# Kernel optimization log

Measured on AMD Instinct MI355X. Metric: run time of the kernel, lower is better.

## Reference

```python
import jax, jax.numpy as jnp
import numpy as np

N_NODES = 4096
N_EDGES = 131072
NUM_USERS = 50000
NUM_ITEMS = 50000
EMB = 64
NUM_CLASSES = 41476
BN_EPS = 1e-5


def _seg_sum(x, idx, n):
    return jax.ops.segment_sum(x, idx, num_segments=n)


def gcn_conv(x, ei, W, b):
    # PyG GCNConv: linear, add self-loops, sym norm D^-1/2 (A+I) D^-1/2, sum-agg, +bias
    n = x.shape[0]
    h = x @ W
    loop = jnp.arange(n, dtype=ei.dtype)
    row = jnp.concatenate([ei[0], loop])
    col = jnp.concatenate([ei[1], loop])
    deg = _seg_sum(jnp.ones_like(col, h.dtype), col, n)
    dinv = jnp.where(deg > 0, deg ** -0.5, 0.0)
    norm = dinv[row] * dinv[col]
    return _seg_sum(h[row] * norm[:, None], col, n) + b


def sage_conv(x, ei, Wl, bl, Wr):
    # PyG SAGEConv (mean aggr): mean_neighbors(x) @ Wl + bl + x @ Wr
    n = x.shape[0]
    ones = jnp.ones((ei.shape[1],), x.dtype)
    cnt = _seg_sum(ones, ei[1], n)
    agg = _seg_sum(x[ei[0]], ei[1], n) / jnp.maximum(cnt, 1.0)[:, None]
    return agg @ Wl + bl + x @ Wr


def cheb_conv(x, ei, W0, W1, b):
    # PyG ChebConv K=2, sym norm, lambda_max=2: L_hat = L - I = -D^-1/2 A D^-1/2
    # out = x @ W0 + (L_hat x) @ W1 + b
    n = x.shape[0]
    ones = jnp.ones((ei.shape[1],), x.dtype)
    deg = _seg_sum(ones, ei[0], n)  # row-sum degree (get_laplacian)
    dinv = jnp.where(deg > 0, deg ** -0.5, 0.0)
    w = -(dinv[ei[0]] * dinv[ei[1]])
    tx1 = _seg_sum(x[ei[0]] * w[:, None], ei[1], n)
    return x @ W0 + tx1 @ W1 + b


def gat_conv(x, ei, W, a_src, a_dst, b):
    # PyG GATConv heads=1, concat=False, self-loops added, leaky_relu(0.2) + softmax over in-edges
    n = x.shape[0]
    h = x @ W
    loop = jnp.arange(n, dtype=ei.dtype)
    row = jnp.concatenate([ei[0], loop])
    col = jnp.concatenate([ei[1], loop])
    a_s = h @ a_src  # [n]
    a_d = h @ a_dst
    e = jax.nn.leaky_relu(a_s[row] + a_d[col], 0.2)
    emax = jax.ops.segment_max(e, col, num_segments=n)  # every segment nonempty (self-loops)
    ex = jnp.exp(e - emax[col])
    denom = _seg_sum(ex, col, n)
    alpha = ex / denom[col]
    return _seg_sum(h[row] * alpha[:, None], col, n) + b


def batch_norm(x, g, be):
    mu = jnp.mean(x, axis=0)
    var = jnp.var(x, axis=0)
    return (x - mu) * jax.lax.rsqrt(var + BN_EPS) * g + be


def setup_inputs() -> dict:
    key = jax.random.key(0)
    ks = iter(jax.random.split(key, 48))
    nrm = lambda shape, s=0.05: jax.random.normal(next(ks), shape, jnp.float32) * s
    edge_index = jax.random.randint(next(ks), (2, N_EDGES), 0, N_NODES, jnp.int32)
    node_x = jax.random.randint(next(ks), (N_NODES, 2), 0, NUM_USERS, jnp.int32)
    inp = dict(
        edge_index=edge_index, node_x=node_x,
        user_emb_w=nrm((NUM_USERS, EMB)), item_emb_w=nrm((NUM_ITEMS, EMB)),
        mlp_w1=nrm((2 * EMB, 1024)), mlp_b1=jnp.zeros((1024,), jnp.float32),
        mlp_w2=nrm((1024, 512)), mlp_b2=jnp.zeros((512,), jnp.float32),
        gcn_w1=nrm((512, 256)), gcn_b1=jnp.zeros((256,), jnp.float32),
        bn1_g=jnp.ones((256,), jnp.float32), bn1_b=jnp.zeros((256,), jnp.float32),
        gcn_w2=nrm((256, 128)), gcn_b2=jnp.zeros((128,), jnp.float32),
        bn2_g=jnp.ones((128,), jnp.float32), bn2_b=jnp.zeros((128,), jnp.float32),
        sage_wl=nrm((128, 128)), sage_bl=jnp.zeros((128,), jnp.float32), sage_wr=nrm((128, 128)),
        cheb_w0=nrm((128, 128)), cheb_w1=nrm((128, 128)), cheb_b=jnp.zeros((128,), jnp.float32),
        gat1_w=nrm((128, 128)), gat1_asrc=nrm((128,)), gat1_adst=nrm((128,)), gat1_b=jnp.zeros((128,), jnp.float32),
        gat2_w=nrm((128, 128)), gat2_asrc=nrm((128,)), gat2_adst=nrm((128,)), gat2_b=jnp.zeros((128,), jnp.float32),
        pred_w=nrm((128, NUM_CLASSES)), pred_b=jnp.zeros((NUM_CLASSES,), jnp.float32),
    )
    return inp


def reference(edge_index, node_x, user_emb_w, item_emb_w, mlp_w1, mlp_b1, mlp_w2, mlp_b2,
              gcn_w1, gcn_b1, bn1_g, bn1_b, gcn_w2, gcn_b2, bn2_g, bn2_b,
              sage_wl, sage_bl, sage_wr, cheb_w0, cheb_w1, cheb_b,
              gat1_w, gat1_asrc, gat1_adst, gat1_b, gat2_w, gat2_asrc, gat2_adst, gat2_b,
              pred_w, pred_b):
    u = user_emb_w[node_x[:, 0]]
    i = item_emb_w[node_x[:, 1]]
    x = jnp.concatenate([u, i], axis=1)  # [N, 2*EMB]
    x = jax.nn.relu(x @ mlp_w1 + mlp_b1)  # dropout = identity (eval mode)
    x = jax.nn.relu(x @ mlp_w2 + mlp_b2)
    x = jax.nn.relu(batch_norm(gcn_conv(x, edge_index, gcn_w1, gcn_b1), bn1_g, bn1_b))
    x = jax.nn.relu(batch_norm(gcn_conv(x, edge_index, gcn_w2, gcn_b2), bn2_g, bn2_b))
    x = jax.nn.relu(sage_conv(x, edge_index, sage_wl, sage_bl, sage_wr))
    x = jax.nn.relu(cheb_conv(x, edge_index, cheb_w0, cheb_w1, cheb_b))
    x = jax.nn.elu(gat_conv(x, edge_index, gat1_w, gat1_asrc, gat1_adst, gat1_b))
    x = jax.nn.elu(gat_conv(x, edge_index, gat2_w, gat2_asrc, gat2_adst, gat2_b))
    return x @ pred_w + pred_b  # [N, NUM_CLASSES]
```

## Files before the change

### kernel.cpp

```cpp
#include <hip/hip_runtime.h>
#include <math.h>

#define NN 4096
#define NE 131072
#define NCLS 41476
#define NPAD 41600

typedef __attribute__((ext_vector_type(8))) unsigned short ushort8;
typedef __attribute__((ext_vector_type(8))) __bf16 bf16x8;
typedef __attribute__((ext_vector_type(4))) float f32x4;

__device__ __forceinline__ unsigned short f2bf(float f) {
  unsigned u = __float_as_uint(f);
  unsigned r = u + 0x7fffu + ((u >> 16) & 1u);
  return (unsigned short)(r >> 16);
}
__device__ __forceinline__ float bf2f(unsigned short u) {
  return __uint_as_float(((unsigned)u) << 16);
}

struct CvtDesc { const float* src; unsigned short* dst; int K, N, ld, koff, tile0, ntx; };
struct CvtArgs { CvtDesc d[11]; };

__global__ void k_fused0(CvtArgs a, int cvtBlocks, const int* __restrict__ ei,
                         int* __restrict__ deg0, int* __restrict__ deg1,
                         const int* __restrict__ node_x, const float* __restrict__ uw,
                         const float* __restrict__ iw, unsigned short* __restrict__ x0) {
  int b = blockIdx.x;
  int tid = threadIdx.x;
  if (b < cvtBlocks) {
    __shared__ float s[32][33];
    int di = 0;
#pragma unroll
    for (int i = 1; i < 11; i++)
      if (a.d[i].tile0 <= b) di = i;
    const CvtDesc dd = a.d[di];
    int t = b - dd.tile0;
    int n0 = (t % dd.ntx) * 32, k0 = (t / dd.ntx) * 32;
    int c = tid & 31, r8 = tid >> 5;
#pragma unroll
    for (int r = 0; r < 4; r++) {
      int k = k0 + r8 + r * 8, n = n0 + c;
      s[r8 + r * 8][c] = (n < dd.N) ? dd.src[(size_t)k * dd.N + n] : 0.f;
    }
    __syncthreads();
#pragma unroll
    for (int r = 0; r < 4; r++) {
      int n = n0 + r8 + r * 8, k = k0 + c;
      dd.dst[(size_t)n * dd.ld + dd.koff + k] = f2bf(s[c][r8 + r * 8]);
    }
  } else if (b < cvtBlocks + 512) {
    int bid = b - cvtBlocks;
    for (int i = bid * 256 + tid; i < 2 * NE; i += 512 * 256) {
      int v = ei[i];
      atomicAdd((i < NE ? deg0 : deg1) + v, 1);
    }
  } else {
    int nb = b - cvtBlocks - 512;
    int n = nb * 2 + (tid >> 7);
    int t = tid & 127;
    int u = node_x[n * 2], it = node_x[n * 2 + 1];
    float v = (t < 64) ? uw[u * 64 + t] : iw[it * 64 + (t - 64)];
    x0[n * 128 + t] = f2bf(v);
  }
}

template <int OUTBF>
__global__ __launch_bounds__(256) void k_bgemm(const unsigned short* __restrict__ A,
                                               const unsigned short* __restrict__ Bt,
                                               const float* __restrict__ bias,
                                               void* __restrict__ Cv, int N, int K, int relu) {
  __shared__ unsigned short As[128 * 128];
  __shared__ unsigned short Bs[128 * 128];
  int m0 = blockIdx.y * 128;
  int n0 = blockIdx.x * 128;
  int tid = threadIdx.x;
  int wave = tid >> 6, lane = tid & 63;
  int wm = (wave >> 1) * 64, wn = (wave & 1) * 64;
  int lr = lane & 15, lg = lane >> 4;
  f32x4 acc[4][4] = {};
  for (int k0 = 0; k0 < K; k0 += 128) {
#pragma unroll
    for (int i = 0; i < 8; i++) {
      int idx = tid + i * 256;
      int row = idx >> 4, ku = idx & 15;
      int sw = (ku ^ (row & 7)) * 8;
      *reinterpret_cast<ushort8*>(As + row * 128 + sw) =
          *reinterpret_cast<const ushort8*>(A + (size_t)(m0 + row) * K + k0 + ku * 8);
      *reinterpret_cast<ushort8*>(Bs + row * 128 + sw) =
          *reinterpret_cast<const ushort8*>(Bt + (size_t)(n0 + row) * K + k0 + ku * 8);
    }
    __syncthreads();
#pragma unroll
    for (int kk = 0; kk < 4; kk++) {
      bf16x8 af[4], bfr[4];
#pragma unroll
      for (int mi = 0; mi < 4; mi++) {
        int row = wm + mi * 16 + lr;
        af[mi] = __builtin_bit_cast(
            bf16x8, *reinterpret_cast<const ushort8*>(As + row * 128 + (((kk * 4 + lg) ^ (row & 7)) * 8)));
        int col = wn + mi * 16 + lr;
        bfr[mi] = __builtin_bit_cast(
            bf16x8, *reinterpret_cast<const ushort8*>(Bs + col * 128 + (((kk * 4 + lg) ^ (col & 7)) * 8)));
      }
#pragma unroll
      for (int mi = 0; mi < 4; mi++)
#pragma unroll
        for (int ni = 0; ni < 4; ni++)
          acc[mi][ni] = __builtin_amdgcn_mfma_f32_16x16x32_bf16(af[mi], bfr[ni], acc[mi][ni], 0, 0, 0);
    }
    __syncthreads();
  }
#pragma unroll
  for (int mi = 0; mi < 4; mi++) {
#pragma unroll
    for (int ni = 0; ni < 4; ni++) {
      int col = n0 + wn + ni * 16 + lr;
      if (col < N) {
        float bv = bias ? bias[col] : 0.f;
#pragma unroll
        for (int r = 0; r < 4; r++) {
          int row = m0 + wm + mi * 16 + lg * 4 + r;
          float v = acc[mi][ni][r] + bv;
          if (relu) v = fmaxf(v, 0.f);
          if (OUTBF)
            ((unsigned short*)Cv)[(size_t)row * N + col] = f2bf(v);
          else
            ((float*)Cv)[(size_t)row * N + col] = v;
        }
      }
    }
  }
}

__global__ __launch_bounds__(256) void k_pred_gemm(const unsigned short* __restrict__ A,
                                                   const unsigned short* __restrict__ Bt,
                                                   const float* __restrict__ bias,
                                                   float* __restrict__ C) {
  __shared__ unsigned short As[128 * 128];
  __shared__ unsigned short Bs[128 * 128];
  int n0 = blockIdx.x * 128;
  int tid = threadIdx.x;
  int wave = tid >> 6, lane = tid & 63;
  int wm = (wave >> 1) * 64, wn = (wave & 1) * 64;
  int lr = lane & 15, lg = lane >> 4;
#pragma unroll
  for (int i = 0; i < 8; i++) {
    int idx = tid + i * 256;
    int row = idx >> 4, ku = idx & 15;
    int sw = (ku ^ (row & 7)) * 8;
    *reinterpret_cast<ushort8*>(Bs + row * 128 + sw) =
        *reinterpret_cast<const ushort8*>(Bt + (size_t)(n0 + row) * 128 + ku * 8);
  }
  float bv[4];
  int colv[4];
#pragma unroll
  for (int ni = 0; ni < 4; ni++) {
    colv[ni] = n0 + wn + ni * 16 + lr;
    bv[ni] = (colv[ni] < NCLS) ? bias[colv[ni]] : 0.f;
  }
  int mt0 = blockIdx.y * 8;
  for (int mt = mt0; mt < mt0 + 8; ++mt) {
    int m0 = mt * 128;
    __syncthreads();
#pragma unroll
    for (int i = 0; i < 8; i++) {
      int idx = tid + i * 256;
      int row = idx >> 4, ku = idx & 15;
      int sw = (ku ^ (row & 7)) * 8;
      *reinterpret_cast<ushort8*>(As + row * 128 + sw) =
          *reinterpret_cast<const ushort8*>(A + (size_t)(m0 + row) * 128 + ku * 8);
    }
    __syncthreads();
    f32x4 acc[4][4] = {};
#pragma unroll
    for (int kk = 0; kk < 4; kk++) {
      bf16x8 af[4], bfr[4];
#pragma unroll
      for (int mi = 0; mi < 4; mi++) {
        int row = wm + mi * 16 + lr;
        af[mi] = __builtin_bit_cast(
            bf16x8, *reinterpret_cast<const ushort8*>(As + row * 128 + (((kk * 4 + lg) ^ (row & 7)) * 8)));
        int col = wn + mi * 16 + lr;
        bfr[mi] = __builtin_bit_cast(
            bf16x8, *reinterpret_cast<const ushort8*>(Bs + col * 128 + (((kk * 4 + lg) ^ (col & 7)) * 8)));
      }
#pragma unroll
      for (int mi = 0; mi < 4; mi++)
#pragma unroll
        for (int ni = 0; ni < 4; ni++)
          acc[mi][ni] = __builtin_amdgcn_mfma_f32_16x16x32_bf16(af[mi], bfr[ni], acc[mi][ni], 0, 0, 0);
    }
#pragma unroll
    for (int mi = 0; mi < 4; mi++) {
#pragma unroll
      for (int ni = 0; ni < 4; ni++) {
        if (colv[ni] < NCLS) {
#pragma unroll
          for (int r = 0; r < 4; r++) {
            int row = m0 + wm + mi * 16 + lg * 4 + r;
            C[(size_t)row * NCLS + colv[ni]] = acc[mi][ni][r] + bv[ni];
          }
        }
      }
    }
  }
}

template <int MODE>
__global__ __launch_bounds__(256) void k_bgemm_s(const void* __restrict__ Av,
                                                 const unsigned short* __restrict__ Bt,
                                                 const float* __restrict__ bias,
                                                 unsigned short* __restrict__ C, int ldC,
                                                 int K, int relu,
                                                 const float* __restrict__ psum,
                                                 const float* __restrict__ psq,
                                                 const float* __restrict__ bng,
                                                 const float* __restrict__ bnb,
                                                 const float* __restrict__ asrc,
                                                 const float* __restrict__ adst,
                                                 float* __restrict__ o_as,
                                                 float* __restrict__ o_ad) {
  __shared__ unsigned short As[32 * 64];
  __shared__ unsigned short Bs[128 * 64];
  __shared__ float sc[256], sh[256];
  __shared__ float sas[4][32], sad[4][32];
  int m0 = blockIdx.y * 32;
  int n0 = blockIdx.x * 128;
  int tid = threadIdx.x;
  int wave = tid >> 6, lane = tid & 63;
  int wn = wave * 32;
  int lr = lane & 15, lg = lane >> 4;
  if (MODE == 1) {
    if (tid < K) {
      int S = 16384 / K;
      float s = 0.f, s2 = 0.f;
      for (int i = 0; i < S; i++) {
        s += psum[(size_t)i * K + tid];
        s2 += psq[(size_t)i * K + tid];
      }
      float invM = 1.f / (float)NN;
      float mu = s * invM;
      float var = s2 * invM - mu * mu;
      float scv = bng[tid] * rsqrtf(var + 1e-5f);
      sc[tid] = scv;
      sh[tid] = bnb[tid] - mu * scv;
    }
    __syncthreads();
  }
  f32x4 acc[2][2] = {};
  for (int k0 = 0; k0 < K; k0 += 64) {
    {
      int row = tid >> 3, uu = tid & 7, sw = (uu ^ (row & 7)) * 8;
      if (MODE == 1) {
        const float* Af = (const float*)Av;
        const float* p = Af + (size_t)(m0 + row) * K + k0 + uu * 8;
        float4 p0 = *reinterpret_cast<const float4*>(p);
        float4 p1 = *reinterpret_cast<const float4*>(p + 4);
        int kb = k0 + uu * 8;
        float pv[8] = {p0.x, p0.y, p0.z, p0.w, p1.x, p1.y, p1.z, p1.w};
        ushort8 o;
#pragma unroll
        for (int j = 0; j < 8; j++) o[j] = f2bf(fmaxf(pv[j] * sc[kb + j] + sh[kb + j], 0.f));
        *reinterpret_cast<ushort8*>(As + row * 64 + sw) = o;
      } else {
        *reinterpret_cast<ushort8*>(As + row * 64 + sw) =
            *reinterpret_cast<const ushort8*>((const unsigned short*)Av + (size_t)(m0 + row) * K + k0 + uu * 8);
      }
    }
#pragma unroll
    for (int i = 0; i < 4; i++) {
      int idx = tid + i * 256;
      int row = idx >> 3, uu = idx & 7, sw = (uu ^ (row & 7)) * 8;
      *reinterpret_cast<ushort8*>(Bs + row * 64 + sw) =
          *reinterpret_cast<const ushort8*>(Bt + (size_t)(n0 + row) * K + k0 + uu * 8);
    }
    __syncthreads();
#pragma unroll
    for (int kk = 0; kk < 2; kk++) {
      bf16x8 af[2], bfr[2];
#pragma unroll
      for (int mi = 0; mi < 2; mi++) {
        int row = mi * 16 + lr;
        af[mi] = __builtin_bit_cast(
            bf16x8, *reinterpret_cast<const ushort8*>(As + row * 64 + (((kk * 4 + lg) ^ (row & 7)) * 8)));
        int col = wn + mi * 16 + lr;
        bfr[mi] = __builtin_bit_cast(
            bf16x8, *reinterpret_cast<const ushort8*>(Bs + col * 64 + (((kk * 4 + lg) ^ (col & 7)) * 8)));
      }
#pragma unroll
      for (int mi = 0; mi < 2; mi++)
#pragma unroll
        for (int ni = 0; ni < 2; ni++)
          acc[mi][ni] = __builtin_amdgcn_mfma_f32_16x16x32_bf16(af[mi], bfr[ni], acc[mi][ni], 0, 0, 0);
    }
    __syncthreads();
  }
  float dss[2][4] = {}, dsd[2][4] = {};
#pragma unroll
  for (int mi = 0; mi < 2; mi++) {
#pragma unroll
    for (int ni = 0; ni < 2; ni++) {
      int col = n0 + wn + ni * 16 + lr;
      float bv = bias ? bias[col] : 0.f;
      float ac = (MODE == 2) ? asrc[col] : 0.f;
      float dc = (MODE == 2) ? adst[col] : 0.f;
#pragma unroll
      for (int r = 0; r < 4; r++) {
        int row = m0 + mi * 16 + lg * 4 + r;
        float v = acc[mi][ni][r] + bv;
        if (relu) v = fmaxf(v, 0.f);
        C[(size_t)row * ldC + col] = f2bf(v);
        if (MODE == 2) { dss[mi][r] += v * ac; dsd[mi][r] += v * dc; }
      }
    }
  }
  if (MODE == 2) {
#pragma unroll
    for (int mi = 0; mi < 2; mi++)
#pragma unroll
      for (int r = 0; r < 4; r++) {
#pragma unroll
        for (int mask = 1; mask < 16; mask <<= 1) {
          dss[mi][r] += __shfl_xor(dss[mi][r], mask);
          dsd[mi][r] += __shfl_xor(dsd[mi][r], mask);
        }
        if (lr == 0) {
          int rowloc = mi * 16 + lg * 4 + r;
          sas[wave][rowloc] = dss[mi][r];
          sad[wave][rowloc] = dsd[mi][r];
        }
      }
    __syncthreads();
    if (tid < 32) {
      float s = sas[0][tid] + sas[1][tid] + sas[2][tid] + sas[3][tid];
      float d = sad[0][tid] + sad[1][tid] + sad[2][tid] + sad[3][tid];
      o_as[m0 + tid] = s;
      o_ad[m0 + tid] = d;
    }
  }
}

__global__ void k_scan4096(const int* __restrict__ deg1, const int* __restrict__ deg0,
                           int* __restrict__ rowptr, int* __restrict__ cursor,
                           float* __restrict__ dinvA, float* __restrict__ dinv0) {
  __shared__ int s[1024];
  int t = threadIdx.x;
  int4 d = *reinterpret_cast<const int4*>(deg1 + t * 4);
  float4 dv = {rsqrtf((float)(d.x + 1)), rsqrtf((float)(d.y + 1)),
               rsqrtf((float)(d.z + 1)), rsqrtf((float)(d.w + 1))};
  *reinterpret_cast<float4*>(dinvA + t * 4) = dv;
  int4 d0 = *reinterpret_cast<const int4*>(deg0 + t * 4);
  float4 dv0 = {d0.x > 0 ? rsqrtf((float)d0.x) : 0.f, d0.y > 0 ? rsqrtf((float)d0.y) : 0.f,
                d0.z > 0 ? rsqrtf((float)d0.z) : 0.f, d0.w > 0 ? rsqrtf((float)d0.w) : 0.f};
  *reinterpret_cast<float4*>(dinv0 + t * 4) = dv0;
  int sum = d.x + d.y + d.z + d.w;
  s[t] = sum;
  __syncthreads();
  for (int off = 1; off < 1024; off <<= 1) {
    int x = (t >= off) ? s[t - off] : 0;
    __syncthreads();
    s[t] += x;
    __syncthreads();
  }
  int base = s[t] - sum;
  int4 o;
  o.x = base; o.y = base + d.x; o.z = o.y + d.y; o.w = o.z + d.z;
  *reinterpret_cast<int4*>(rowptr + t * 4) = o;
  *reinterpret_cast<int4*>(cursor + t * 4) = o;
  if (t == 1023) rowptr[4096] = base + sum;
}

__global__ void k_fill(const int* __restrict__ ei0, const int* __restrict__ ei1,
                       int* __restrict__ cursor, int* __restrict__ csr_src) {
  int e = blockIdx.x * blockDim.x + threadIdx.x;
  if (e < NE) {
    int pos = atomicAdd(&cursor[ei1[e]], 1);
    csr_src[pos] = ei0[e];
  }
}

template <int VEC>
__global__ void k_gcn_agg(const unsigned short* __restrict__ h, const int* __restrict__ rowptr,
                          const int* __restrict__ csr_src, const float* __restrict__ dinv,
                          float* __restrict__ out) {
  constexpr int F = 64 * VEC;
  __shared__ int sld[128];
  __shared__ float wld[128];
  __shared__ float red[3][64 * VEC];
  int c = blockIdx.x, tid = threadIdx.x, wv = tid >> 6, ln = tid & 63;
  float dc = dinv[c];
  int r0 = rowptr[c], r1 = rowptr[c + 1];
  float acc[VEC] = {};
  for (int base = r0; base < r1; base += 128) {
    int nb = min(128, r1 - base);
    __syncthreads();
    if (tid < nb) { int s = csr_src[base + tid]; sld[tid] = s; wld[tid] = dinv[s]; }
    __syncthreads();
    for (int i = wv; i < nb; i += 4) {
      float w = wld[i];
      const unsigned short* p = h + (size_t)sld[i] * F + ln * VEC;
      if (VEC == 2) {
        ushort2 v = *reinterpret_cast<const ushort2*>(p);
        acc[0] += bf2f(v.x) * w; acc[1] += bf2f(v.y) * w;
      } else {
        ushort4 v = *reinterpret_cast<const ushort4*>(p);
        acc[0] += bf2f(v.x) * w; acc[1] += bf2f(v.y) * w;
        acc[2] += bf2f(v.z) * w; acc[3] += bf2f(v.w) * w;
      }
    }
  }
  if (wv) {
#pragma unroll
    for (int j = 0; j < VEC; j++) red[wv - 1][ln * VEC + j] = acc[j];
  }
  __syncthreads();
  if (wv == 0) {
    const unsigned short* pc = h + (size_t)c * F + ln * VEC;
#pragma unroll
    for (int j = 0; j < VEC; j++) {
      acc[j] += red[0][ln * VEC + j] + red[1][ln * VEC + j] + red[2][ln * VEC + j];
      acc[j] += bf2f(pc[j]) * dc;
      out[(size_t)c * F + ln * VEC + j] = acc[j] * dc;
    }
  }
}

__global__ void k_sage_agg(const unsigned short* __restrict__ x, const int* __restrict__ rowptr,
                           const int* __restrict__ csr_src, unsigned short* __restrict__ out) {
  __shared__ int sld[128];
  __shared__ float red[3][128];
  int c = blockIdx.x, tid = threadIdx.x, wv = tid >> 6, ln = tid & 63;
  int r0 = rowptr[c], r1 = rowptr[c + 1];
  float a0 = 0.f, a1 = 0.f;
  for (int base = r0; base < r1; base += 128) {
    int nb = min(128, r1 - base);
    __syncthreads();
    if (tid < nb) sld[tid] = csr_src[base + tid];
    __syncthreads();
    for (int i = wv; i < nb; i += 4) {
      ushort2 v = *reinterpret_cast<const ushort2*>(x + (size_t)sld[i] * 256 + ln * 2);
      a0 += bf2f(v.x); a1 += bf2f(v.y);
    }
  }
  if (wv) { red[wv - 1][ln * 2] = a0; red[wv - 1][ln * 2 + 1] = a1; }
  __syncthreads();
  if (wv == 0) {
    a0 += red[0][ln * 2] + red[1][ln * 2] + red[2][ln * 2];
    a1 += red[0][ln * 2 + 1] + red[1][ln * 2 + 1] + red[2][ln * 2 + 1];
    float inv = 1.f / fmaxf((float)(r1 - r0), 1.f);
    ushort2 o; o.x = f2bf(a0 * inv); o.y = f2bf(a1 * inv);
    *reinterpret_cast<ushort2*>(out + (size_t)c * 256 + ln * 2) = o;
  }
}

__global__ void k_cheb_agg(const unsigned short* __restrict__ x, const int* __restrict__ rowptr,
                           const int* __restrict__ csr_src, const float* __restrict__ dinv0,
                           unsigned short* __restrict__ out) {
  __shared__ int sld[128];
  __shared__ float wld[128];
  __shared__ float red[3][128];
  int c = blockIdx.x, tid = threadIdx.x, wv = tid >> 6, ln = tid & 63;
  int r0 = rowptr[c], r1 = rowptr[c + 1];
  float a0 = 0.f, a1 = 0.f;
  for (int base = r0; base < r1; base += 128) {
    int nb = min(128, r1 - base);
    __syncthreads();
    if (tid < nb) { int s = csr_src[base + tid]; sld[tid] = s; wld[tid] = dinv0[s]; }
    __syncthreads();
    for (int i = wv; i < nb; i += 4) {
      float w = wld[i];
      ushort2 v = *reinterpret_cast<const ushort2*>(x + (size_t)sld[i] * 256 + ln * 2);
      a0 += bf2f(v.x) * w; a1 += bf2f(v.y) * w;
    }
  }
  if (wv) { red[wv - 1][ln * 2] = a0; red[wv - 1][ln * 2 + 1] = a1; }
  __syncthreads();
  if (wv == 0) {
    a0 += red[0][ln * 2] + red[1][ln * 2] + red[2][ln * 2];
    a1 += red[0][ln * 2 + 1] + red[1][ln * 2 + 1] + red[2][ln * 2 + 1];
    float s = -dinv0[c];
    ushort2 o; o.x = f2bf(a0 * s); o.y = f2bf(a1 * s);
    *reinterpret_cast<ushort2*>(out + (size_t)c * 256 + ln * 2) = o;
  }
}

__global__ void k_gat_agg(const unsigned short* __restrict__ h, const int* __restrict__ rowptr,
                          const int* __restrict__ csr_src, const float* __restrict__ a_s,
                          const float* __restrict__ a_d, const float* __restrict__ bias,
                          unsigned short* __restrict__ out) {
  __shared__ int sld[128];
  __shared__ float eld[128];
  __shared__ float red[3][128];
  __shared__ float sden[4];
  __shared__ float smax[256];
  int c = blockIdx.x, tid = threadIdx.x, wv = tid >> 6, ln = tid & 63;
  int r0 = rowptr[c], r1 = rowptr[c + 1];
  float adc = a_d[c];
  float es = a_s[c] + adc;
  es = es >= 0.f ? es : 0.2f * es;
  float m = es;
  for (int i = r0 + tid; i < r1; i += 256) {
    float v = a_s[csr_src[i]] + adc;
    m = fmaxf(m, v >= 0.f ? v : 0.2f * v);
  }
  smax[tid] = m;
  __syncthreads();
  for (int sft = 128; sft; sft >>= 1) {
    if (tid < sft) smax[tid] = fmaxf(smax[tid], smax[tid + sft]);
    __syncthreads();
  }
  m = smax[0];
  float a0 = 0.f, a1 = 0.f, den = 0.f;
  for (int base = r0; base < r1; base += 128) {
    int nb = min(128, r1 - base);
    __syncthreads();
    if (tid < nb) {
      int s = csr_src[base + tid];
      sld[tid] = s;
      float v = a_s[s] + adc;
      v = v >= 0.f ? v : 0.2f * v;
      eld[tid] = expf(v - m);
    }
    __syncthreads();
    for (int i = wv; i < nb; i += 4) {
      float w = eld[i];
      den += w;
      ushort2 v = *reinterpret_cast<const ushort2*>(h + (size_t)sld[i] * 128 + ln * 2);
      a0 += w * bf2f(v.x); a1 += w * bf2f(v.y);
    }
  }
  if (wv) {
    red[wv - 1][ln * 2] = a0; red[wv - 1][ln * 2 + 1] = a1;
    if (ln == 0) sden[wv] = den;
  }
  __syncthreads();
  if (wv == 0) {
    a0 += red[0][ln * 2] + red[1][ln * 2] + red[2][ln * 2];
    a1 += red[0][ln * 2 + 1] + red[1][ln * 2 + 1] + red[2][ln * 2 + 1];
    den += sden[1] + sden[2] + sden[3];
    float ws = expf(es - m);
    den += ws;
    ushort2 xc = *reinterpret_cast<const ushort2*>(h + (size_t)c * 128 + ln * 2);
    a0 += ws * bf2f(xc.x); a1 += ws * bf2f(xc.y);
    float inv = 1.f / den;
    float v0 = a0 * inv + bias[ln * 2];
    float v1 = a1 * inv + bias[ln * 2 + 1];
    v0 = v0 > 0.f ? v0 : expm1f(v0);
    v1 = v1 > 0.f ? v1 : expm1f(v1);
    ushort2 o; o.x = f2bf(v0); o.y = f2bf(v1);
    *reinterpret_cast<ushort2*>(out + (size_t)c * 128 + ln * 2) = o;
  }
}

__global__ void k_bn_stats(const float* __restrict__ x, float* __restrict__ psum,
                           float* __restrict__ psq, int F) {
  int tid = threadIdx.x;
  int f = tid & (F - 1);
  int rstep = 256 / F;
  int r0 = tid / F;
  int base = blockIdx.x * 64;
  float s = 0.f, s2 = 0.f;
  for (int rr = r0; rr < 64; rr += rstep) {
    float v = x[(size_t)(base + rr) * F + f];
    s += v;
    s2 += v * v;
  }
  int slot = blockIdx.x * rstep + r0;
  psum[(size_t)slot * F + f] = s;
  psq[(size_t)slot * F + f] = s2;
}

__global__ void k_bn_apply2(const float* __restrict__ x, const float* __restrict__ psum,
                            const float* __restrict__ psq, const float* __restrict__ g,
                            const float* __restrict__ be, unsigned short* __restrict__ y,
                            int ldY) {
  __shared__ float sc[128], sh[128];
  int tid = threadIdx.x;
  if (tid < 128) {
    float s = 0.f, s2 = 0.f;
    for (int i = 0; i < 128; i++) {
      s += psum[(size_t)i * 128 + tid];
      s2 += psq[(size_t)i * 128 + tid];
    }
    float invM = 1.f / (float)NN;
    float mu = s * invM;
    float var = s2 * invM - mu * mu;
    float scv = g[tid] * rsqrtf(var + 1e-5f);
    sc[tid] = scv;
    sh[tid] = be[tid] - mu * scv;
  }
  __syncthreads();
  int f = tid & 127, rhalf = tid >> 7;
  int row0 = blockIdx.x * 16;
  for (int rr = 0; rr < 8; rr++) {
    int row = row0 + rr * 2 + rhalf;
    float v = fmaxf(x[(size_t)row * 128 + f] * sc[f] + sh[f], 0.f);
    y[(size_t)row * ldY + f] = f2bf(v);
  }
}

static inline int cdiv(int a, int b) { return (a + b - 1) / b; }

extern "C" void kernel_launch(void* const* d_in, const int* in_sizes, int n_in,
                              void* d_out, int out_size, void* d_ws, size_t ws_size,
                              hipStream_t stream) {
  const int* ei = (const int*)d_in[0];
  const int* ei0 = ei;
  const int* ei1 = ei + NE;
  const int* node_x = (const int*)d_in[1];
  const float* user_w = (const float*)d_in[2];
  const float* item_w = (const float*)d_in[3];
  const float* mlp_w1 = (const float*)d_in[4];
  const float* mlp_b1 = (const float*)d_in[5];
  const float* mlp_w2 = (const float*)d_in[6];
  const float* mlp_b2 = (const float*)d_in[7];
  const float* gcn_w1 = (const float*)d_in[8];
  const float* bn1_g = (const float*)d_in[10];
  const float* bn1_b = (const float*)d_in[11];
  const float* gcn_w2 = (const float*)d_in[12];
  const float* bn2_g = (const float*)d_in[14];
  const float* bn2_b = (const float*)d_in[15];
  const float* sage_wl = (const float*)d_in[16];
  const float* sage_bl = (const float*)d_in[17];
  const float* sage_wr = (const float*)d_in[18];
  const float* cheb_w0 = (const float*)d_in[19];
  const float* cheb_w1 = (const float*)d_in[20];
  const float* cheb_b = (const float*)d_in[21];
  const float* gat1_w = (const float*)d_in[22];
  const float* gat1_as = (const float*)d_in[23];
  const float* gat1_ad = (const float*)d_in[24];
  const float* gat1_b = (const float*)d_in[25];
  const float* gat2_w = (const float*)d_in[26];
  const float* gat2_as = (const float*)d_in[27];
  const float* gat2_ad = (const float*)d_in[28];
  const float* gat2_b = (const float*)d_in[29];
  const float* pred_w = (const float*)d_in[30];
  const float* pred_b = (const float*)d_in[31];

  char* w = (char*)d_ws;
  size_t off = 0;
  auto alloc = [&](size_t bytes) -> char* {
    char* p = w + off;
    off = (off + bytes + 255) & ~(size_t)255;
    return p;
  };
  unsigned short* x0b = (unsigned short*)alloc((size_t)NN * 128 * 2);
  unsigned short* x1b = (unsigned short*)alloc((size_t)NN * 1024 * 2);
  unsigned short* x2b = (unsigned short*)alloc((size_t)NN * 512 * 2);
  unsigned short* h1b = (unsigned short*)alloc((size_t)NN * 256 * 2);
  unsigned short* catS = (unsigned short*)alloc((size_t)NN * 256 * 2);
  unsigned short* catC = (unsigned short*)alloc((size_t)NN * 256 * 2);
  unsigned short* xb2 = (unsigned short*)alloc((size_t)NN * 128 * 2);
  unsigned short* hb = (unsigned short*)alloc((size_t)NN * 128 * 2);
  unsigned short* xa2 = (unsigned short*)alloc((size_t)NN * 128 * 2);
  unsigned short* xb3 = (unsigned short*)alloc((size_t)NN * 128 * 2);
  float* agg = (float*)alloc((size_t)NN * 256 * 4);
  unsigned short* w1t = (unsigned short*)alloc((size_t)1024 * 128 * 2);
  unsigned short* w2t = (unsigned short*)alloc((size_t)512 * 1024 * 2);
  unsigned short* g1t = (unsigned short*)alloc((size_t)256 * 512 * 2);
  unsigned short* g2t = (unsigned short*)alloc((size_t)128 * 256 * 2);
  unsigned short* sgt = (unsigned short*)alloc((size_t)128 * 256 * 2);
  unsigned short* cht = (unsigned short*)alloc((size_t)128 * 256 * 2);
  unsigned short* a1t = (unsigned short*)alloc((size_t)128 * 128 * 2);
  unsigned short* a2t = (unsigned short*)alloc((size_t)128 * 128 * 2);
  unsigned short* predT = (unsigned short*)alloc((size_t)NPAD * 128 * 2);
  int* deg0 = (int*)alloc(NN * 4);
  int* deg1 = (int*)alloc(NN * 4);
  int* rowptr = (int*)alloc((NN + 1) * 4);
  int* cursor = (int*)alloc(NN * 4);
  int* csr_src = (int*)alloc(NE * 4);
  float* dinvA = (float*)alloc(NN * 4);
  float* dinv0 = (float*)alloc(NN * 4);
  float* a_s = (float*)alloc(NN * 4);
  float* a_d = (float*)alloc(NN * 4);
  float* psum = (float*)alloc(16384 * 4);
  float* psq = (float*)alloc(16384 * 4);

  CvtArgs ca;
  int t0 = 0;
  auto mkd = [&](int i, const float* src, unsigned short* dst, int K, int N, int ld, int koff,
                 int ntx) {
    ca.d[i] = {src, dst, K, N, ld, koff, t0, ntx};
    t0 += ntx * (K / 32);
  };
  mkd(0, mlp_w1, w1t, 128, 1024, 128, 0, 32);
  mkd(1, mlp_w2, w2t, 1024, 512, 1024, 0, 16);
  mkd(2, gcn_w1, g1t, 512, 256, 512, 0, 8);
  mkd(3, gcn_w2, g2t, 256, 128, 256, 0, 4);
  mkd(4, sage_wl, sgt, 128, 128, 256, 0, 4);
  mkd(5, sage_wr, sgt, 128, 128, 256, 128, 4);
  mkd(6, cheb_w0, cht, 128, 128, 256, 0, 4);
  mkd(7, cheb_w1, cht, 128, 128, 256, 128, 4);
  mkd(8, gat1_w, a1t, 128, 128, 128, 0, 4);
  mkd(9, gat2_w, a2t, 128, 128, 128, 0, 4);
  mkd(10, pred_w, predT, 128, NCLS, 128, 0, NPAD / 32);

  hipMemsetAsync(deg0, 0, 2 * NN * 4, stream);
  k_fused0<<<t0 + 512 + NN / 2, 256, 0, stream>>>(ca, t0, ei, deg0, deg1, node_x, user_w,
                                                  item_w, x0b);
  k_scan4096<<<1, 1024, 0, stream>>>(deg1, deg0, rowptr, cursor, dinvA, dinv0);
  k_fill<<<cdiv(NE, 256), 256, 0, stream>>>(ei0, ei1, cursor, csr_src);

  k_bgemm<1><<<dim3(8, 32), 256, 0, stream>>>(x0b, w1t, mlp_b1, x1b, 1024, 128, 1);
  k_bgemm<1><<<dim3(4, 32), 256, 0, stream>>>(x1b, w2t, mlp_b2, x2b, 512, 1024, 1);

  k_bgemm_s<0><<<dim3(2, 128), 256, 0, stream>>>(x2b, g1t, nullptr, h1b, 256, 512, 0,
                                                 nullptr, nullptr, nullptr, nullptr, nullptr,
                                                 nullptr, nullptr, nullptr);
  k_gcn_agg<4><<<NN, 256, 0, stream>>>(h1b, rowptr, csr_src, dinvA, agg);
  k_bn_stats<<<64, 256, 0, stream>>>(agg, psum, psq, 256);

  k_bgemm_s<1><<<dim3(1, 128), 256, 0, stream>>>(agg, g2t, nullptr, hb, 128, 256, 0,
                                                 psum, psq, bn1_g, bn1_b, nullptr, nullptr,
                                                 nullptr, nullptr);
  k_gcn_agg<2><<<NN, 256, 0, stream>>>(hb, rowptr, csr_src, dinvA, agg);
  k_bn_stats<<<64, 256, 0, stream>>>(agg, psum, psq, 128);
  k_bn_apply2<<<256, 256, 0, stream>>>(agg, psum, psq, bn2_g, bn2_b, catS + 128, 256);

  k_sage_agg<<<NN, 256, 0, stream>>>(catS + 128, rowptr, csr_src, catS);
  k_bgemm_s<0><<<dim3(1, 128), 256, 0, stream>>>(catS, sgt, sage_bl, catC, 256, 256, 1,
                                                 nullptr, nullptr, nullptr, nullptr, nullptr,
                                                 nullptr, nullptr, nullptr);

  k_cheb_agg<<<NN, 256, 0, stream>>>(catC, rowptr, csr_src, dinv0, catC + 128);
  k_bgemm_s<0><<<dim3(1, 128), 256, 0, stream>>>(catC, cht, cheb_b, xb2, 128, 256, 1,
                                                 nullptr, nullptr, nullptr, nullptr, nullptr,
                                                 nullptr, nullptr, nullptr);

  k_bgemm_s<2><<<dim3(1, 128), 256, 0, stream>>>(xb2, a1t, nullptr, hb, 128, 128, 0,
                                                 nullptr, nullptr, nullptr, nullptr,
                                                 gat1_as, gat1_ad, a_s, a_d);
  k_gat_agg<<<NN, 256, 0, stream>>>(hb, rowptr, csr_src, a_s, a_d, gat1_b, xa2);

  k_bgemm_s<2><<<dim3(1, 128), 256, 0, stream>>>(xa2, a2t, nullptr, hb, 128, 128, 0,
                                                 nullptr, nullptr, nullptr, nullptr,
                                                 gat2_as, gat2_ad, a_s, a_d);
  k_gat_agg<<<NN, 256, 0, stream>>>(hb, rowptr, csr_src, a_s, a_d, gat2_b, xb3);

  k_pred_gemm<<<dim3(NPAD / 128, 4), 256, 0, stream>>>(xb3, predT, pred_b, (float*)d_out);
}
```

Before: 469.9 us.

## Use one wave per node in graph aggregations and prefetch A tiles in pred GEMM

All graph aggregation kernels (GCN, SAGE, Cheb, GAT) now map one 64-lane wave to one destination node, with four nodes per block. This removes the shared-memory staging, block barriers and cross-wave reductions, at the cost of serial per-edge index loads within each wave. The prediction GEMM now register-prefetches the next A tile while computing the current one, and covers 4 M-tiles per block instead of 8, so it launches twice as many blocks. The wave-per-node mapping relies on average degree around 32, so nodes with high degree become long serial loops.

```diff
diff --git a/kernel.cpp b/kernel.cpp
--- a/kernel.cpp
+++ b/kernel.cpp
@@ -159,8 +159,18 @@
     colv[ni] = n0 + wn + ni * 16 + lr;
     bv[ni] = (colv[ni] < NCLS) ? bias[colv[ni]] : 0.f;
   }
-  int mt0 = blockIdx.y * 8;
-  for (int mt = mt0; mt < mt0 + 8; ++mt) {
+  int mt0 = blockIdx.y * 4;
+  ushort8 areg[8];
+  {
+    int m0 = mt0 * 128;
+#pragma unroll
+    for (int i = 0; i < 8; i++) {
+      int idx = tid + i * 256;
+      int row = idx >> 4, ku = idx & 15;
+      areg[i] = *reinterpret_cast<const ushort8*>(A + (size_t)(m0 + row) * 128 + ku * 8);
+    }
+  }
+  for (int mt = mt0; mt < mt0 + 4; ++mt) {
     int m0 = mt * 128;
     __syncthreads();
 #pragma unroll
@@ -168,10 +178,18 @@
       int idx = tid + i * 256;
       int row = idx >> 4, ku = idx & 15;
       int sw = (ku ^ (row & 7)) * 8;
-      *reinterpret_cast<ushort8*>(As + row * 128 + sw) =
-          *reinterpret_cast<const ushort8*>(A + (size_t)(m0 + row) * 128 + ku * 8);
-    }
-    __syncthreads();
+      *reinterpret_cast<ushort8*>(As + row * 128 + sw) = areg[i];
+    }
+    __syncthreads();
+    if (mt + 1 < mt0 + 4) {
+      int m0n = (mt + 1) * 128;
+#pragma unroll
+      for (int i = 0; i < 8; i++) {
+        int idx = tid + i * 256;
+        int row = idx >> 4, ku = idx & 15;
+        areg[i] = *reinterpret_cast<const ushort8*>(A + (size_t)(m0n + row) * 128 + ku * 8);
+      }
+    }
     f32x4 acc[4][4] = {};
 #pragma unroll
     for (int kk = 0; kk < 4; kk++) {
@@ -385,172 +403,112 @@
                           const int* __restrict__ csr_src, const float* __restrict__ dinv,
                           float* __restrict__ out) {
   constexpr int F = 64 * VEC;
-  __shared__ int sld[128];
-  __shared__ float wld[128];
-  __shared__ float red[3][64 * VEC];
-  int c = blockIdx.x, tid = threadIdx.x, wv = tid >> 6, ln = tid & 63;
+  int wv = threadIdx.x >> 6, ln = threadIdx.x & 63;
+  int c = blockIdx.x * 4 + wv;
   float dc = dinv[c];
   int r0 = rowptr[c], r1 = rowptr[c + 1];
-  float acc[VEC] = {};
-  for (int base = r0; base < r1; base += 128) {
-    int nb = min(128, r1 - base);
-    __syncthreads();
-    if (tid < nb) { int s = csr_src[base + tid]; sld[tid] = s; wld[tid] = dinv[s]; }
-    __syncthreads();
-    for (int i = wv; i < nb; i += 4) {
-      float w = wld[i];
-      const unsigned short* p = h + (size_t)sld[i] * F + ln * VEC;
-      if (VEC == 2) {
-        ushort2 v = *reinterpret_cast<const ushort2*>(p);
-        acc[0] += bf2f(v.x) * w; acc[1] += bf2f(v.y) * w;
-      } else {
-        ushort4 v = *reinterpret_cast<const ushort4*>(p);
-        acc[0] += bf2f(v.x) * w; acc[1] += bf2f(v.y) * w;
-        acc[2] += bf2f(v.z) * w; acc[3] += bf2f(v.w) * w;
-      }
-    }
-  }
-  if (wv) {
-#pragma unroll
-    for (int j = 0; j < VEC; j++) red[wv - 1][ln * VEC + j] = acc[j];
-  }
-  __syncthreads();
-  if (wv == 0) {
+  float acc[VEC];
+  {
     const unsigned short* pc = h + (size_t)c * F + ln * VEC;
-#pragma unroll
-    for (int j = 0; j < VEC; j++) {
-      acc[j] += red[0][ln * VEC + j] + red[1][ln * VEC + j] + red[2][ln * VEC + j];
-      acc[j] += bf2f(pc[j]) * dc;
-      out[(size_t)c * F + ln * VEC + j] = acc[j] * dc;
-    }
+    if (VEC == 2) {
+      ushort2 v = *reinterpret_cast<const ushort2*>(pc);
+      acc[0] = bf2f(v.x) * dc; acc[1] = bf2f(v.y) * dc;
+    } else {
+      ushort4 v = *reinterpret_cast<const ushort4*>(pc);
+      acc[0] = bf2f(v.x) * dc; acc[1] = bf2f(v.y) * dc;
+      acc[2] = bf2f(v.z) * dc; acc[3] = bf2f(v.w) * dc;
+    }
+  }
+  for (int i = r0; i < r1; i++) {
+    int s = csr_src[i];
+    float w = dinv[s];
+    const unsigned short* p = h + (size_t)s * F + ln * VEC;
+    if (VEC == 2) {
+      ushort2 v = *reinterpret_cast<const ushort2*>(p);
+      acc[0] += bf2f(v.x) * w; acc[1] += bf2f(v.y) * w;
+    } else {
+      ushort4 v = *reinterpret_cast<const ushort4*>(p);
+      acc[0] += bf2f(v.x) * w; acc[1] += bf2f(v.y) * w;
+      acc[2] += bf2f(v.z) * w; acc[3] += bf2f(v.w) * w;
+    }
+  }
+  if (VEC == 2) {
+    float2 o = {acc[0] * dc, acc[1] * dc};
+    *reinterpret_cast<float2*>(out + (size_t)c * F + ln * 2) = o;
+  } else {
+    float4 o = {acc[0] * dc, acc[1] * dc, acc[2] * dc, acc[3] * dc};
+    *reinterpret_cast<float4*>(out + (size_t)c * F + ln * 4) = o;
   }
 }
 
 __global__ void k_sage_agg(const unsigned short* __restrict__ x, const int* __restrict__ rowptr,
                            const int* __restrict__ csr_src, unsigned short* __restrict__ out) {
-  __shared__ int sld[128];
-  __shared__ float red[3][128];
-  int c = blockIdx.x, tid = threadIdx.x, wv = tid >> 6, ln = tid & 63;
+  int wv = threadIdx.x >> 6, ln = threadIdx.x & 63;
+  int c = blockIdx.x * 4 + wv;
   int r0 = rowptr[c], r1 = rowptr[c + 1];
   float a0 = 0.f, a1 = 0.f;
-  for (int base = r0; base < r1; base += 128) {
-    int nb = min(128, r1 - base);
-    __syncthreads();
-    if (tid < nb) sld[tid] = csr_src[base + tid];
-    __syncthreads();
-    for (int i = wv; i < nb; i += 4) {
-      ushort2 v = *reinterpret_cast<const ushort2*>(x + (size_t)sld[i] * 256 + ln * 2);
-      a0 += bf2f(v.x); a1 += bf2f(v.y);
-    }
-  }
-  if (wv) { red[wv - 1][ln * 2] = a0; red[wv - 1][ln * 2 + 1] = a1; }
-  __syncthreads();
-  if (wv == 0) {
-    a0 += red[0][ln * 2] + red[1][ln * 2] + red[2][ln * 2];
-    a1 += red[0][ln * 2 + 1] + red[1][ln * 2 + 1] + red[2][ln * 2 + 1];
-    float inv = 1.f / fmaxf((float)(r1 - r0), 1.f);
-    ushort2 o; o.x = f2bf(a0 * inv); o.y = f2bf(a1 * inv);
-    *reinterpret_cast<ushort2*>(out + (size_t)c * 256 + ln * 2) = o;
-  }
+  for (int i = r0; i < r1; i++) {
+    int s = csr_src[i];
+    ushort2 v = *reinterpret_cast<const ushort2*>(x + (size_t)s * 256 + ln * 2);
+    a0 += bf2f(v.x); a1 += bf2f(v.y);
+  }
+  float inv = 1.f / fmaxf((float)(r1 - r0), 1.f);
+  ushort2 o; o.x = f2bf(a0 * inv); o.y = f2bf(a1 * inv);
+  *reinterpret_cast<ushort2*>(out + (size_t)c * 256 + ln * 2) = o;
 }
 
 __global__ void k_cheb_agg(const unsigned short* __restrict__ x, const int* __restrict__ rowptr,
                            const int* __restrict__ csr_src, const float* __restrict__ dinv0,
                            unsigned short* __restrict__ out) {
-  __shared__ int sld[128];
-  __shared__ float wld[128];
-  __shared__ float red[3][128];
-  int c = blockIdx.x, tid = threadIdx.x, wv = tid >> 6, ln = tid & 63;
+  int wv = threadIdx.x >> 6, ln = threadIdx.x & 63;
+  int c = blockIdx.x * 4 + wv;
   int r0 = rowptr[c], r1 = rowptr[c + 1];
   float a0 = 0.f, a1 = 0.f;
-  for (int base = r0; base < r1; base += 128) {
-    int nb = min(128, r1 - base);
-    __syncthreads();
-    if (tid < nb) { int s = csr_src[base + tid]; sld[tid] = s; wld[tid] = dinv0[s]; }
-    __syncthreads();
-    for (int i = wv; i < nb; i += 4) {
-      float w = wld[i];
-      ushort2 v = *reinterpret_cast<const ushort2*>(x + (size_t)sld[i] * 256 + ln * 2);
-      a0 += bf2f(v.x) * w; a1 += bf2f(v.y) * w;
-    }
-  }
-  if (wv) { red[wv - 1][ln * 2] = a0; red[wv - 1][ln * 2 + 1] = a1; }
-  __syncthreads();
-  if (wv == 0) {
-    a0 += red[0][ln * 2] + red[1][ln * 2] + red[2][ln * 2];
-    a1 += red[0][ln * 2 + 1] + red[1][ln * 2 + 1] + red[2][ln * 2 + 1];
-    float s = -dinv0[c];
-    ushort2 o; o.x = f2bf(a0 * s); o.y = f2bf(a1 * s);
-    *reinterpret_cast<ushort2*>(out + (size_t)c * 256 + ln * 2) = o;
-  }
+  for (int i = r0; i < r1; i++) {
+    int s = csr_src[i];
+    float w = dinv0[s];
+    ushort2 v = *reinterpret_cast<const ushort2*>(x + (size_t)s * 256 + ln * 2);
+    a0 += bf2f(v.x) * w; a1 += bf2f(v.y) * w;
+  }
+  float sgn = -dinv0[c];
+  ushort2 o; o.x = f2bf(a0 * sgn); o.y = f2bf(a1 * sgn);
+  *reinterpret_cast<ushort2*>(out + (size_t)c * 256 + ln * 2) = o;
 }
 
 __global__ void k_gat_agg(const unsigned short* __restrict__ h, const int* __restrict__ rowptr,
                           const int* __restrict__ csr_src, const float* __restrict__ a_s,
                           const float* __restrict__ a_d, const float* __restrict__ bias,
                           unsigned short* __restrict__ out) {
-  __shared__ int sld[128];
-  __shared__ float eld[128];
-  __shared__ float red[3][128];
-  __shared__ float sden[4];
-  __shared__ float smax[256];
-  int c = blockIdx.x, tid = threadIdx.x, wv = tid >> 6, ln = tid & 63;
+  int wv = threadIdx.x >> 6, ln = threadIdx.x & 63;
+  int c = blockIdx.x * 4 + wv;
   int r0 = rowptr[c], r1 = rowptr[c + 1];
   float adc = a_d[c];
   float es = a_s[c] + adc;
   es = es >= 0.f ? es : 0.2f * es;
   float m = es;
-  for (int i = r0 + tid; i < r1; i += 256) {
+  for (int i = r0; i < r1; i++) {
     float v = a_s[csr_src[i]] + adc;
     m = fmaxf(m, v >= 0.f ? v : 0.2f * v);
   }
-  smax[tid] = m;
-  __syncthreads();
-  for (int sft = 128; sft; sft >>= 1) {
-    if (tid < sft) smax[tid] = fmaxf(smax[tid], smax[tid + sft]);
-    __syncthreads();
-  }
-  m = smax[0];
-  float a0 = 0.f, a1 = 0.f, den = 0.f;
-  for (int base = r0; base < r1; base += 128) {
-    int nb = min(128, r1 - base);
-    __syncthreads();
-    if (tid < nb) {
-      int s = csr_src[base + tid];
-      sld[tid] = s;
-      float v = a_s[s] + adc;
-      v = v >= 0.f ? v : 0.2f * v;
-      eld[tid] = expf(v - m);
-    }
-    __syncthreads();
-    for (int i = wv; i < nb; i += 4) {
-      float w = eld[i];
-      den += w;
-      ushort2 v = *reinterpret_cast<const ushort2*>(h + (size_t)sld[i] * 128 + ln * 2);
-      a0 += w * bf2f(v.x); a1 += w * bf2f(v.y);
-    }
-  }
-  if (wv) {
-    red[wv - 1][ln * 2] = a0; red[wv - 1][ln * 2 + 1] = a1;
-    if (ln == 0) sden[wv] = den;
-  }
-  __syncthreads();
-  if (wv == 0) {
-    a0 += red[0][ln * 2] + red[1][ln * 2] + red[2][ln * 2];
-    a1 += red[0][ln * 2 + 1] + red[1][ln * 2 + 1] + red[2][ln * 2 + 1];
-    den += sden[1] + sden[2] + sden[3];
-    float ws = expf(es - m);
-    den += ws;
-    ushort2 xc = *reinterpret_cast<const ushort2*>(h + (size_t)c * 128 + ln * 2);
-    a0 += ws * bf2f(xc.x); a1 += ws * bf2f(xc.y);
-    float inv = 1.f / den;
-    float v0 = a0 * inv + bias[ln * 2];
-    float v1 = a1 * inv + bias[ln * 2 + 1];
-    v0 = v0 > 0.f ? v0 : expm1f(v0);
-    v1 = v1 > 0.f ? v1 : expm1f(v1);
-    ushort2 o; o.x = f2bf(v0); o.y = f2bf(v1);
-    *reinterpret_cast<ushort2*>(out + (size_t)c * 128 + ln * 2) = o;
-  }
+  float den = expf(es - m);
+  ushort2 xc = *reinterpret_cast<const ushort2*>(h + (size_t)c * 128 + ln * 2);
+  float a0 = den * bf2f(xc.x), a1 = den * bf2f(xc.y);
+  for (int i = r0; i < r1; i++) {
+    int s = csr_src[i];
+    float v = a_s[s] + adc;
+    v = v >= 0.f ? v : 0.2f * v;
+    float w = expf(v - m);
+    den += w;
+    ushort2 hv = *reinterpret_cast<const ushort2*>(h + (size_t)s * 128 + ln * 2);
+    a0 += w * bf2f(hv.x); a1 += w * bf2f(hv.y);
+  }
+  float inv = 1.f / den;
+  float v0 = a0 * inv + bias[ln * 2];
+  float v1 = a1 * inv + bias[ln * 2 + 1];
+  v0 = v0 > 0.f ? v0 : expm1f(v0);
+  v1 = v1 > 0.f ? v1 : expm1f(v1);
+  ushort2 o; o.x = f2bf(v0); o.y = f2bf(v1);
+  *reinterpret_cast<ushort2*>(out + (size_t)c * 128 + ln * 2) = o;
 }
 
 __global__ void k_bn_stats(const float* __restrict__ x, float* __restrict__ psum,
@@ -708,22 +666,22 @@
   k_bgemm_s<0><<<dim3(2, 128), 256, 0, stream>>>(x2b, g1t, nullptr, h1b, 256, 512, 0,
                                                  nullptr, nullptr, nullptr, nullptr, nullptr,
                                                  nullptr, nullptr, nullptr);
-  k_gcn_agg<4><<<NN, 256, 0, stream>>>(h1b, rowptr, csr_src, dinvA, agg);
+  k_gcn_agg<4><<<NN / 4, 256, 0, stream>>>(h1b, rowptr, csr_src, dinvA, agg);
   k_bn_stats<<<64, 256, 0, stream>>>(agg, psum, psq, 256);
 
   k_bgemm_s<1><<<dim3(1, 128), 256, 0, stream>>>(agg, g2t, nullptr, hb, 128, 256, 0,
                                                  psum, psq, bn1_g, bn1_b, nullptr, nullptr,
                                                  nullptr, nullptr);
-  k_gcn_agg<2><<<NN, 256, 0, stream>>>(hb, rowptr, csr_src, dinvA, agg);
+  k_gcn_agg<2><<<NN / 4, 256, 0, stream>>>(hb, rowptr, csr_src, dinvA, agg);
   k_bn_stats<<<64, 256, 0, stream>>>(agg, psum, psq, 128);
   k_bn_apply2<<<256, 256, 0, stream>>>(agg, psum, psq, bn2_g, bn2_b, catS + 128, 256);
 
-  k_sage_agg<<<NN, 256, 0, stream>>>(catS + 128, rowptr, csr_src, catS);
+  k_sage_agg<<<NN / 4, 256, 0, stream>>>(catS + 128, rowptr, csr_src, catS);
   k_bgemm_s<0><<<dim3(1, 128), 256, 0, stream>>>(catS, sgt, sage_bl, catC, 256, 256, 1,
                                                  nullptr, nullptr, nullptr, nullptr, nullptr,
                                                  nullptr, nullptr, nullptr);
 
-  k_cheb_agg<<<NN, 256, 0, stream>>>(catC, rowptr, csr_src, dinv0, catC + 128);
+  k_cheb_agg<<<NN / 4, 256, 0, stream>>>(catC, rowptr, csr_src, dinv0, catC + 128);
   k_bgemm_s<0><<<dim3(1, 128), 256, 0, stream>>>(catC, cht, cheb_b, xb2, 128, 256, 1,
                                                  nullptr, nullptr, nullptr, nullptr, nullptr,
                                                  nullptr, nullptr, nullptr);
@@ -731,12 +689,12 @@
   k_bgemm_s<2><<<dim3(1, 128), 256, 0, stream>>>(xb2, a1t, nullptr, hb, 128, 128, 0,
                                                  nullptr, nullptr, nullptr, nullptr,
                                                  gat1_as, gat1_ad, a_s, a_d);
-  k_gat_agg<<<NN, 256, 0, stream>>>(hb, rowptr, csr_src, a_s, a_d, gat1_b, xa2);
+  k_gat_agg<<<NN / 4, 256, 0, stream>>>(hb, rowptr, csr_src, a_s, a_d, gat1_b, xa2);
 
   k_bgemm_s<2><<<dim3(1, 128), 256, 0, stream>>>(xa2, a2t, nullptr, hb, 128, 128, 0,
                                                  nullptr, nullptr, nullptr, nullptr,
                                                  gat2_as, gat2_ad, a_s, a_d);
-  k_gat_agg<<<NN, 256, 0, stream>>>(hb, rowptr, csr_src, a_s, a_d, gat2_b, xb3);
-
-  k_pred_gemm<<<dim3(NPAD / 128, 4), 256, 0, stream>>>(xb3, predT, pred_b, (float*)d_out);
-}
+  k_gat_agg<<<NN / 4, 256, 0, stream>>>(hb, rowptr, csr_src, a_s, a_d, gat2_b, xb3);
+
+  k_pred_gemm<<<dim3(NPAD / 128, 8), 256, 0, stream>>>(xb3, predT, pred_b, (float*)d_out);
+}
```

Result: slower. 523.3 us (+11.3%).
